# Optimization experiments

Hardware: AMD Instinct MI355X
Metric: run time of the kernel (lower is better)

The kernel has to match this reference:

```python
import jax, jax.numpy as jnp
import numpy as np

TAU_S = 5.0  # network_config['tau_s']; n_steps inferred from trailing dim


def psp(x, tau_s):
    """Leaky synaptic integrator along the last (time) axis.
    x: [B, C, H, W, T] -> syns: [B, C, H, W, T]
    syn_t = syn_{t-1} * (1 - 1/tau_s) + x_t ;  out_t = syn_t / tau_s
    """
    decay = 1.0 - 1.0 / tau_s
    xt = jnp.moveaxis(x, -1, 0)  # [T, B, C, H, W]

    def step(syn, inp):
        syn = syn * decay + inp
        return syn, syn / tau_s

    _, ys = jax.lax.scan(step, jnp.zeros_like(xt[0]), xt)
    return jnp.moveaxis(ys, 0, -1)  # [B, C, H, W, T]


def setup_inputs() -> dict:
    key = jax.random.key(0)
    k1, k2 = jax.random.split(key)
    B, C, H, W, T = 32, 256, 4, 4, 100
    outputs = jax.random.normal(k1, (B, C, H, W, T), dtype=jnp.float32)
    # target is a spike train in the original; uniform [0,1) floats keep the
    # same math and dtype (fill='rand' per input_specs)
    target = jax.random.uniform(k2, (B, C, H, W, T), dtype=jnp.float32)
    return {"outputs": outputs, "target": target}


def reference(outputs, target):
    # spike_kernel: delta = outputs - psp(target); loss = 0.5 * sum(delta^2)
    delta = outputs - psp(target, TAU_S)
    return 0.5 * jnp.sum(delta * delta)
```

## Files before the change

kernel.cpp:

```cpp
#include <hip/hip_runtime.h>


#define T_DIM 100
#define BLOCK 256

__global__ __launch_bounds__(BLOCK) void spike_loss_kernel(
    const float* __restrict__ outs, const float* __restrict__ tgt,
    float* __restrict__ loss, int P) {
  const float DECAY = 0.8f;
  const float INV_TAU = 0.2f;

  int row = blockIdx.x * BLOCK + threadIdx.x;
  float acc = 0.0f;

  if (row < P) {
    const float4* o4 = reinterpret_cast<const float4*>(outs + (size_t)row * T_DIM);
    const float4* t4 = reinterpret_cast<const float4*>(tgt + (size_t)row * T_DIM);
    float syn = 0.0f;
#pragma unroll 5
    for (int k = 0; k < T_DIM / 4; ++k) {
      float4 o = o4[k];
      float4 t = t4[k];
      float d;
      syn = syn * DECAY + t.x; d = o.x - syn * INV_TAU; acc += d * d;
      syn = syn * DECAY + t.y; d = o.y - syn * INV_TAU; acc += d * d;
      syn = syn * DECAY + t.z; d = o.z - syn * INV_TAU; acc += d * d;
      syn = syn * DECAY + t.w; d = o.w - syn * INV_TAU; acc += d * d;
    }
  }

#pragma unroll
  for (int off = 32; off > 0; off >>= 1) acc += __shfl_down(acc, off, 64);

  __shared__ float wave_sums[BLOCK / 64];
  int lane = threadIdx.x & 63;
  int wid = threadIdx.x >> 6;
  if (lane == 0) wave_sums[wid] = acc;
  __syncthreads();

  if (threadIdx.x == 0) {
    float s = 0.0f;
#pragma unroll
    for (int w = 0; w < BLOCK / 64; ++w) s += wave_sums[w];
    atomicAdd(loss, 0.5f * s);
  }
}

extern "C" void kernel_launch(void* const* d_in, const int* in_sizes, int n_in,
                              void* d_out, int out_size, void* d_ws, size_t ws_size,
                              hipStream_t stream) {
  const float* outputs = (const float*)d_in[0];
  const float* target  = (const float*)d_in[1];
  float* loss = (float*)d_out;

  int P = in_sizes[0] / T_DIM;

  hipMemsetAsync(d_out, 0, sizeof(float), stream);

  dim3 grid((P + BLOCK - 1) / BLOCK);
  hipLaunchKernelGGL(spike_loss_kernel, grid, dim3(BLOCK), 0, stream,
                     outputs, target, loss, P);
}
```

Baseline: 142.6 us.

## Stage rows in LDS and split time recurrence into four chunks algebraically

Each block now loads 64 rows of outputs and targets into shared memory with coalesced float4 reads, instead of each thread streaming its own 400-byte row. The 100-step recurrence is split into four 25-step chunks handled by four threads. Each chunk first runs from a zero initial state, and the squared error is then corrected with closed-form alpha/beta/gamma terms that use the carried-in synaptic state gathered by shuffles. This targets uncoalesced per-thread global access and the long serial dependency chain. In exchange it uses about 51 KB of LDS per block, which limits occupancy, and it changes the floating-point summation order slightly.

```diff
diff --git a/kernel.cpp b/kernel.cpp
--- a/kernel.cpp
+++ b/kernel.cpp
@@ -2,47 +2,94 @@
 
 
 #define T_DIM 100
+#define ROWS   64
 #define BLOCK 256
+#define CHUNK  25
+
+constexpr float DECAY   = 0.8f;
+constexpr float INV_TAU = 0.2f;
+
+constexpr float compute_gamma() {
+  double g = 0.0, p = 0.2 * 0.8;
+  for (int k = 0; k < CHUNK; ++k) { g += p * p; p *= 0.8; }
+  return (float)g;
+}
+constexpr float compute_d25() {
+  double p = 1.0;
+  for (int k = 0; k < CHUNK; ++k) p *= 0.8;
+  return (float)p;
+}
+constexpr float GAMMA = compute_gamma();
+constexpr float D25   = compute_d25();
 
 __global__ __launch_bounds__(BLOCK) void spike_loss_kernel(
     const float* __restrict__ outs, const float* __restrict__ tgt,
     float* __restrict__ loss, int P) {
-  const float DECAY = 0.8f;
-  const float INV_TAU = 0.2f;
+  __shared__ float lo[ROWS * T_DIM];
+  __shared__ float lx[ROWS * T_DIM];
 
-  int row = blockIdx.x * BLOCK + threadIdx.x;
-  float acc = 0.0f;
+  const int t = threadIdx.x;
+  const int row0 = blockIdx.x * ROWS;
+  const int vrows = min(ROWS, P - row0);
+  const int nf4 = vrows * (T_DIM / 4);
 
-  if (row < P) {
-    const float4* o4 = reinterpret_cast<const float4*>(outs + (size_t)row * T_DIM);
-    const float4* t4 = reinterpret_cast<const float4*>(tgt + (size_t)row * T_DIM);
-    float syn = 0.0f;
-#pragma unroll 5
-    for (int k = 0; k < T_DIM / 4; ++k) {
-      float4 o = o4[k];
-      float4 t = t4[k];
-      float d;
-      syn = syn * DECAY + t.x; d = o.x - syn * INV_TAU; acc += d * d;
-      syn = syn * DECAY + t.y; d = o.y - syn * INV_TAU; acc += d * d;
-      syn = syn * DECAY + t.z; d = o.z - syn * INV_TAU; acc += d * d;
-      syn = syn * DECAY + t.w; d = o.w - syn * INV_TAU; acc += d * d;
+  const size_t base_f = (size_t)row0 * T_DIM;
+  const float4* og = reinterpret_cast<const float4*>(outs + base_f);
+  const float4* xg = reinterpret_cast<const float4*>(tgt + base_f);
+  float4* lo4 = reinterpret_cast<float4*>(lo);
+  float4* lx4 = reinterpret_cast<float4*>(lx);
+
+  for (int j = t; j < nf4; j += BLOCK) {
+    lo4[j] = og[j];
+    lx4[j] = xg[j];
+  }
+  __syncthreads();
+
+  const int r = t >> 2;
+  const int c = t & 3;
+
+  float alpha = 0.f, beta = 0.f, s = 0.f;
+  if (r < vrows) {
+    const float* po = lo + r * T_DIM + c * CHUNK;
+    const float* px = lx + r * T_DIM + c * CHUNK;
+    float B = INV_TAU * DECAY;
+#pragma unroll
+    for (int k = 0; k < CHUNK; ++k) {
+      s = s * DECAY + px[k];
+      float A = fmaf(-INV_TAU, s, po[k]);
+      alpha = fmaf(A, A, alpha);
+      beta  = fmaf(A, B, beta);
+      B *= DECAY;
     }
   }
+
+  const int lane = t & 63;
+  const int g = lane & ~3;
+  float sA = __shfl(s, g + 0, 64);
+  float sB = __shfl(s, g + 1, 64);
+  float sC = __shfl(s, g + 2, 64);
+  float w0 = (c == 1) ? 1.f : (c == 2) ? D25 : (c == 3) ? D25 * D25 : 0.f;
+  float w1 = (c == 2) ? 1.f : (c == 3) ? D25 : 0.f;
+  float w2 = (c == 3) ? 1.f : 0.f;
+  float syn_in = sA * w0 + sB * w1 + sC * w2;
+
+  float acc = (r < vrows)
+      ? alpha - 2.f * beta * syn_in + GAMMA * syn_in * syn_in
+      : 0.f;
 
 #pragma unroll
   for (int off = 32; off > 0; off >>= 1) acc += __shfl_down(acc, off, 64);
 
   __shared__ float wave_sums[BLOCK / 64];
-  int lane = threadIdx.x & 63;
-  int wid = threadIdx.x >> 6;
+  const int wid = t >> 6;
   if (lane == 0) wave_sums[wid] = acc;
   __syncthreads();
 
-  if (threadIdx.x == 0) {
-    float s = 0.0f;
+  if (t == 0) {
+    float sum = 0.f;
 #pragma unroll
-    for (int w = 0; w < BLOCK / 64; ++w) s += wave_sums[w];
-    atomicAdd(loss, 0.5f * s);
+    for (int w = 0; w < BLOCK / 64; ++w) sum += wave_sums[w];
+    atomicAdd(loss, 0.5f * sum);
   }
 }
 
@@ -57,7 +104,7 @@
 
   hipMemsetAsync(d_out, 0, sizeof(float), stream);
 
-  dim3 grid((P + BLOCK - 1) / BLOCK);
+  dim3 grid((P + ROWS - 1) / ROWS);
   hipLaunchKernelGGL(spike_loss_kernel, grid, dim3(BLOCK), 0, stream,
                      outputs, target, loss, P);
 }
```

New measurement: 133.4 us. 1.07x faster.

## Parallelize time recurrence with wave-level scan and closed-form segment loss

Applied to the files above, without the earlier changes.

Replaces the one-thread-per-row sequential scan with a layout where each lane handles four time steps of a row, two rows per wavefront of 50 active lanes. It propagates the synaptic state across lanes with a log-step decayed prefix scan and computes each segment's loss in closed form from local sums and the carried-in state. This makes the loads fully coalesced and shortens the serial dependency chain. The single atomic is replaced by per-block partials plus a second reduction kernel. In exchange, 14 of 64 lanes sit idle and the grid and row count are hard-coded to the test shape, with float rounding changes from the algebraic expansion.

```diff
diff --git a/kernel.cpp b/kernel.cpp
--- a/kernel.cpp
+++ b/kernel.cpp
@@ -2,62 +2,107 @@
 
 
 #define T_DIM 100
-#define BLOCK 256
+#define BLOCK1 1024
+#define GRID1  4096
+#define NPART  GRID1
 
-__global__ __launch_bounds__(BLOCK) void spike_loss_kernel(
-    const float* __restrict__ outs, const float* __restrict__ tgt,
-    float* __restrict__ loss, int P) {
-  const float DECAY = 0.8f;
-  const float INV_TAU = 0.2f;
+constexpr double D  = 0.8;
+constexpr double D4 = D * D * D * D;
+constexpr float K1  = (float)D4;
+constexpr float K2  = (float)(D4 * D4);
+constexpr float K4  = (float)(D4 * D4 * D4 * D4);
+constexpr float K8  = (float)(D4*D4*D4*D4*D4*D4*D4*D4);
+constexpr float K16 = (float)(D4*D4*D4*D4*D4*D4*D4*D4*D4*D4*D4*D4*D4*D4*D4*D4);
 
-  int row = blockIdx.x * BLOCK + threadIdx.x;
-  float acc = 0.0f;
+constexpr float B0 = 0.2f * 0.8f;
+constexpr float B1 = 0.2f * 0.8f * 0.8f;
+constexpr float B2 = 0.2f * 0.8f * 0.8f * 0.8f;
+constexpr float B3 = 0.2f * 0.8f * 0.8f * 0.8f * 0.8f;
+constexpr float G4 = B0*B0 + B1*B1 + B2*B2 + B3*B3;
 
-  if (row < P) {
-    const float4* o4 = reinterpret_cast<const float4*>(outs + (size_t)row * T_DIM);
-    const float4* t4 = reinterpret_cast<const float4*>(tgt + (size_t)row * T_DIM);
-    float syn = 0.0f;
-#pragma unroll 5
-    for (int k = 0; k < T_DIM / 4; ++k) {
-      float4 o = o4[k];
-      float4 t = t4[k];
-      float d;
-      syn = syn * DECAY + t.x; d = o.x - syn * INV_TAU; acc += d * d;
-      syn = syn * DECAY + t.y; d = o.y - syn * INV_TAU; acc += d * d;
-      syn = syn * DECAY + t.z; d = o.z - syn * INV_TAU; acc += d * d;
-      syn = syn * DECAY + t.w; d = o.w - syn * INV_TAU; acc += d * d;
-    }
+__global__ __launch_bounds__(BLOCK1) void spike_loss_partial(
+    const float4* __restrict__ o4g, const float4* __restrict__ x4g,
+    float* __restrict__ parts) {
+  const int t    = threadIdx.x;
+  const int lane = t & 63;
+  const int gw   = blockIdx.x * (BLOCK1 / 64) + (t >> 6);
+  const bool active = lane < 50;
+  const int seg = (lane < 25) ? lane : lane - 25;
+
+  float abar = 0.f, bbar = 0.f, s = 0.f;
+  if (active) {
+    const int j = gw * 50 + lane;
+    float4 o = o4g[j];
+    float4 x = x4g[j];
+    float u, a;
+    u = x.x;                 a = fmaf(-0.2f, u, o.x);
+    abar = a * a;            bbar = a * B0;
+    u = fmaf(0.8f, u, x.y);  a = fmaf(-0.2f, u, o.y);
+    abar = fmaf(a, a, abar); bbar = fmaf(a, B1, bbar);
+    u = fmaf(0.8f, u, x.z);  a = fmaf(-0.2f, u, o.z);
+    abar = fmaf(a, a, abar); bbar = fmaf(a, B2, bbar);
+    u = fmaf(0.8f, u, x.w);  a = fmaf(-0.2f, u, o.w);
+    abar = fmaf(a, a, abar); bbar = fmaf(a, B3, bbar);
+    s = u;
   }
 
+  float c = s, up;
+  up = __shfl_up(c, 1, 64);  if (seg >= 1)  c = fmaf(K1,  up, c);
+  up = __shfl_up(c, 2, 64);  if (seg >= 2)  c = fmaf(K2,  up, c);
+  up = __shfl_up(c, 4, 64);  if (seg >= 4)  c = fmaf(K4,  up, c);
+  up = __shfl_up(c, 8, 64);  if (seg >= 8)  c = fmaf(K8,  up, c);
+  up = __shfl_up(c, 16, 64); if (seg >= 16) c = fmaf(K16, up, c);
+  up = __shfl_up(c, 1, 64);
+  float sigma = (seg > 0) ? up : 0.f;
+
+  float loss = active
+      ? fmaf(G4 * sigma - 2.f * bbar, sigma, abar)
+      : 0.f;
+
 #pragma unroll
-  for (int off = 32; off > 0; off >>= 1) acc += __shfl_down(acc, off, 64);
+  for (int off = 32; off > 0; off >>= 1) loss += __shfl_down(loss, off, 64);
 
-  __shared__ float wave_sums[BLOCK / 64];
-  int lane = threadIdx.x & 63;
-  int wid = threadIdx.x >> 6;
-  if (lane == 0) wave_sums[wid] = acc;
+  __shared__ float wsum[BLOCK1 / 64];
+  if (lane == 0) wsum[t >> 6] = loss;
   __syncthreads();
+  if (t < 64) {
+    float v = (t < BLOCK1 / 64) ? wsum[t] : 0.f;
+#pragma unroll
+    for (int off = 8; off > 0; off >>= 1) v += __shfl_down(v, off, 64);
+    if (t == 0) parts[blockIdx.x] = v;
+  }
+}
 
-  if (threadIdx.x == 0) {
-    float s = 0.0f;
+__global__ __launch_bounds__(1024) void spike_loss_final(
+    const float* __restrict__ parts, float* __restrict__ out) {
+  const int t = threadIdx.x;
+  float v = 0.f;
 #pragma unroll
-    for (int w = 0; w < BLOCK / 64; ++w) s += wave_sums[w];
-    atomicAdd(loss, 0.5f * s);
+  for (int i = 0; i < NPART / 1024; ++i) v += parts[t + i * 1024];
+#pragma unroll
+  for (int off = 32; off > 0; off >>= 1) v += __shfl_down(v, off, 64);
+
+  __shared__ float wsum[16];
+  if ((t & 63) == 0) wsum[t >> 6] = v;
+  __syncthreads();
+  if (t == 0) {
+    float sum = 0.f;
+#pragma unroll
+    for (int w = 0; w < 16; ++w) sum += wsum[w];
+    *out = 0.5f * sum;
   }
 }
 
 extern "C" void kernel_launch(void* const* d_in, const int* in_sizes, int n_in,
                               void* d_out, int out_size, void* d_ws, size_t ws_size,
                               hipStream_t stream) {
-  const float* outputs = (const float*)d_in[0];
-  const float* target  = (const float*)d_in[1];
-  float* loss = (float*)d_out;
+  const float4* o4 = (const float4*)d_in[0];
+  const float4* x4 = (const float4*)d_in[1];
+  float* parts = (float*)d_ws;
+  float* loss  = (float*)d_out;
 
-  int P = in_sizes[0] / T_DIM;
-
-  hipMemsetAsync(d_out, 0, sizeof(float), stream);
-
-  dim3 grid((P + BLOCK - 1) / BLOCK);
-  hipLaunchKernelGGL(spike_loss_kernel, grid, dim3(BLOCK), 0, stream,
-                     outputs, target, loss, P);
+  hipLaunchKernelGGL(spike_loss_partial, dim3(GRID1), dim3(BLOCK1), 0, stream,
+                     o4, x4, parts);
+  hipLaunchKernelGGL(spike_loss_final, dim3(1), dim3(1024), 0, stream,
+                     parts, loss);
 }
```

After: 118.3 us. 17.0% less time.

## Parallelize the time scan across lanes with a closed-form carry correction

Applied to the files above, without the earlier changes.

Each row's 100-step recurrence is split across 25 lanes holding 4 timesteps each, and two rows share one 64-lane wavefront, so global float4 loads become contiguous across a wave. The loss is first computed locally, assuming zero carry-in. A decay-weighted shuffle prefix scan then gives each segment's incoming synaptic state, and a precomputed quadratic correction in that carry is applied. This removes the strided per-thread row reads of the old kernel, which coalesced poorly. In exchange, the grid size assumes the input divides evenly into tiles, 14 of 64 lanes sit idle, and the memset of the output was dropped, so correctness depends on the harness zeroing the output.

```diff
diff --git a/kernel.cpp b/kernel.cpp
--- a/kernel.cpp
+++ b/kernel.cpp
@@ -1,63 +1,95 @@
 #include <hip/hip_runtime.h>
 
 
-#define T_DIM 100
-#define BLOCK 256
+#define BLOCK 1024
+#define WPB   (BLOCK / 64)
+#define GTILE 4
+#define TILES 65536
+
+constexpr double dpow(double b, int n) {
+  double r = 1.0; for (int i = 0; i < n; ++i) r *= b; return r;
+}
+constexpr float K1  = (float)dpow(0.4096, 1);
+constexpr float K2  = (float)dpow(0.4096, 2);
+constexpr float K4  = (float)dpow(0.4096, 4);
+constexpr float K8  = (float)dpow(0.4096, 8);
+constexpr float K16 = (float)dpow(0.4096, 16);
+constexpr float B0 = (float)(0.2 * dpow(0.8, 1));
+constexpr float B1 = (float)(0.2 * dpow(0.8, 2));
+constexpr float B2 = (float)(0.2 * dpow(0.8, 3));
+constexpr float B3 = (float)(0.2 * dpow(0.8, 4));
+constexpr float G4C = (float)(0.04 * (dpow(0.8, 2) + dpow(0.8, 4) +
+                                      dpow(0.8, 6) + dpow(0.8, 8)));
 
 __global__ __launch_bounds__(BLOCK) void spike_loss_kernel(
-    const float* __restrict__ outs, const float* __restrict__ tgt,
-    float* __restrict__ loss, int P) {
-  const float DECAY = 0.8f;
-  const float INV_TAU = 0.2f;
+    const float4* __restrict__ o4g, const float4* __restrict__ x4g,
+    float* __restrict__ out) {
+  const int t    = threadIdx.x;
+  const int lane = t & 63;
+  const int w    = t >> 6;
+  const int W    = blockIdx.x * WPB + w;
+  const bool active = lane < 50;
+  const int lidx = active ? lane : 49;
+  const int seg  = (lidx < 25) ? lidx : lidx - 25;
 
-  int row = blockIdx.x * BLOCK + threadIdx.x;
-  float acc = 0.0f;
+  const size_t f4base = (size_t)W * (GTILE * 50) + lidx;
+  const float4* op = o4g + f4base;
+  const float4* xp = x4g + f4base;
 
-  if (row < P) {
-    const float4* o4 = reinterpret_cast<const float4*>(outs + (size_t)row * T_DIM);
-    const float4* t4 = reinterpret_cast<const float4*>(tgt + (size_t)row * T_DIM);
-    float syn = 0.0f;
-#pragma unroll 5
-    for (int k = 0; k < T_DIM / 4; ++k) {
-      float4 o = o4[k];
-      float4 t = t4[k];
-      float d;
-      syn = syn * DECAY + t.x; d = o.x - syn * INV_TAU; acc += d * d;
-      syn = syn * DECAY + t.y; d = o.y - syn * INV_TAU; acc += d * d;
-      syn = syn * DECAY + t.z; d = o.z - syn * INV_TAU; acc += d * d;
-      syn = syn * DECAY + t.w; d = o.w - syn * INV_TAU; acc += d * d;
-    }
+  float4 ov[GTILE], xv[GTILE];
+#pragma unroll
+  for (int g = 0; g < GTILE; ++g) { ov[g] = op[g * 50]; xv[g] = xp[g * 50]; }
+
+  float loss = 0.f;
+#pragma unroll
+  for (int g = 0; g < GTILE; ++g) {
+    float u, a, abar, bbar;
+    u = xv[g].x;                 a = fmaf(-0.2f, u, ov[g].x);
+    abar = a * a;                bbar = a * B0;
+    u = fmaf(0.8f, u, xv[g].y);  a = fmaf(-0.2f, u, ov[g].y);
+    abar = fmaf(a, a, abar);     bbar = fmaf(a, B1, bbar);
+    u = fmaf(0.8f, u, xv[g].z);  a = fmaf(-0.2f, u, ov[g].z);
+    abar = fmaf(a, a, abar);     bbar = fmaf(a, B2, bbar);
+    u = fmaf(0.8f, u, xv[g].w);  a = fmaf(-0.2f, u, ov[g].w);
+    abar = fmaf(a, a, abar);     bbar = fmaf(a, B3, bbar);
+
+    float c = u, up;
+    up = __shfl_up(c, 1, 64);  if (seg >= 1)  c = fmaf(K1,  up, c);
+    up = __shfl_up(c, 2, 64);  if (seg >= 2)  c = fmaf(K2,  up, c);
+    up = __shfl_up(c, 4, 64);  if (seg >= 4)  c = fmaf(K4,  up, c);
+    up = __shfl_up(c, 8, 64);  if (seg >= 8)  c = fmaf(K8,  up, c);
+    up = __shfl_up(c, 16, 64); if (seg >= 16) c = fmaf(K16, up, c);
+    up = __shfl_up(c, 1, 64);
+    float sigma = (seg > 0) ? up : 0.f;
+
+    float contrib = fmaf(G4C * sigma - 2.f * bbar, sigma, abar);
+    loss += active ? contrib : 0.f;
   }
 
 #pragma unroll
-  for (int off = 32; off > 0; off >>= 1) acc += __shfl_down(acc, off, 64);
+  for (int off = 32; off > 0; off >>= 1) loss += __shfl_down(loss, off, 64);
 
-  __shared__ float wave_sums[BLOCK / 64];
-  int lane = threadIdx.x & 63;
-  int wid = threadIdx.x >> 6;
-  if (lane == 0) wave_sums[wid] = acc;
+  __shared__ float wsum[WPB];
+  if (lane == 0) wsum[w] = loss;
   __syncthreads();
-
-  if (threadIdx.x == 0) {
-    float s = 0.0f;
+  if (t < 64) {
+    float v = (t < WPB) ? wsum[t] : 0.f;
 #pragma unroll
-    for (int w = 0; w < BLOCK / 64; ++w) s += wave_sums[w];
-    atomicAdd(loss, 0.5f * s);
+    for (int off = 8; off > 0; off >>= 1) v += __shfl_down(v, off, 64);
+    if (t == 0) atomicAdd(out, 0.5f * v);
   }
 }
 
 extern "C" void kernel_launch(void* const* d_in, const int* in_sizes, int n_in,
                               void* d_out, int out_size, void* d_ws, size_t ws_size,
                               hipStream_t stream) {
-  const float* outputs = (const float*)d_in[0];
-  const float* target  = (const float*)d_in[1];
+  const float4* o4 = (const float4*)d_in[0];
+  const float4* x4 = (const float4*)d_in[1];
   float* loss = (float*)d_out;
 
-  int P = in_sizes[0] / T_DIM;
+  const int tiles = in_sizes[0] / 200;
+  const int grid  = tiles / (WPB * GTILE);
 
-  hipMemsetAsync(d_out, 0, sizeof(float), stream);
-
-  dim3 grid((P + BLOCK - 1) / BLOCK);
-  hipLaunchKernelGGL(spike_loss_kernel, grid, dim3(BLOCK), 0, stream,
-                     outputs, target, loss, P);
+  hipLaunchKernelGGL(spike_loss_kernel, dim3(grid), dim3(BLOCK), 0, stream,
+                     o4, x4, loss);
 }
```

Result: faster. 117.8 us (-17.3%).
